# Kernel tuning notes

Hardware: AMD Instinct MI355X
Metric: run time of the kernel (lower is better)

## Reference

```python
import jax, jax.numpy as jnp
import numpy as np

B, S, D, H = 2, 2048, 1024, 16
HD = D // H


def setup_inputs() -> dict:
    key = jax.random.key(0)
    ks = jax.random.split(key, 7)
    mk = lambda k, shape, scale=1.0: (jax.random.normal(k, shape, dtype=jnp.float32) * scale)
    w_scale = 1.0 / np.sqrt(D)  # ~nn.Linear init scale
    return {
        "query": mk(ks[0], (B, S, D)),
        "key": mk(ks[1], (B, S, D)),
        "value": mk(ks[2], (B, S, D)),
        "Wq": mk(ks[3], (D, D), w_scale),
        "Wk": mk(ks[4], (D, D), w_scale),
        "Wv": mk(ks[5], (D, D), w_scale),
        "Wo": mk(ks[6], (D, D), w_scale),
    }


def reference(query, key, value, Wq, Wk, Wv, Wo):
    # torch nn.Linear(bias=False): y = x @ W.T, W is (out, in)
    def proj(x, W):
        y = jnp.einsum('bsd,ed->bse', x, W)          # [B, S, D]
        return y.reshape(x.shape[0], x.shape[1], H, HD).transpose(0, 2, 1, 3)  # [B, H, S, HD]

    Q = proj(query, Wq)
    K = proj(key, Wk)
    V = proj(value, Wv)

    # NOTE: original scales by sqrt(embedding_size), not sqrt(head_dim)
    scale = 1.0 / jnp.sqrt(jnp.asarray(D, dtype=Q.dtype))
    scores = jnp.einsum('bhqd,bhkd->bhqk', Q, K) * scale   # [B, H, Q, K]
    attn = jax.nn.softmax(scores, axis=-1)
    ctx = jnp.einsum('bhqk,bhkd->bhqd', attn, V)           # [B, H, Q, HD]
    ctx = ctx.transpose(0, 2, 1, 3).reshape(query.shape[0], query.shape[1], D)
    return jnp.einsum('bsd,ed->bse', ctx, Wo)
```

## Files before the change

### kernel.cpp

```cpp
#include <hip/hip_runtime.h>
#include <hip/hip_bf16.h>


typedef __bf16 bf16x8 __attribute__((ext_vector_type(8)));
typedef float f32x2 __attribute__((ext_vector_type(2)));
typedef float f32x4 __attribute__((ext_vector_type(4)));
typedef float f32x8 __attribute__((ext_vector_type(8)));
typedef float f32x16 __attribute__((ext_vector_type(16)));
typedef int i32x4 __attribute__((ext_vector_type(4)));

static constexpr int Bb = 2, Ss = 2048, Dd = 1024, Hh = 16, HDd = 64;
static constexpr int Mtot = Bb * Ss;

__global__ __launch_bounds__(256) void cast_all(
    const float* __restrict__ a0, const float* __restrict__ a1, const float* __restrict__ a2,
    const float* __restrict__ a3, const float* __restrict__ a4, const float* __restrict__ a5,
    const float* __restrict__ a6, __hip_bfloat16* __restrict__ d0, __hip_bfloat16* __restrict__ d1,
    __hip_bfloat16* __restrict__ d2, __hip_bfloat16* __restrict__ d3,
    __hip_bfloat16* __restrict__ d4, __hip_bfloat16* __restrict__ d5,
    __hip_bfloat16* __restrict__ d6, int nact8, int nw8) {
  const float* src;
  __hip_bfloat16* dst;
  int n8;
  switch (blockIdx.y) {
    case 0: src = a0; dst = d0; n8 = nact8; break;
    case 1: src = a1; dst = d1; n8 = nact8; break;
    case 2: src = a2; dst = d2; n8 = nact8; break;
    case 3: src = a3; dst = d3; n8 = nw8; break;
    case 4: src = a4; dst = d4; n8 = nw8; break;
    case 5: src = a5; dst = d5; n8 = nw8; break;
    default: src = a6; dst = d6; n8 = nw8; break;
  }
  int i = blockIdx.x * 256 + threadIdx.x;
  if (i >= n8) return;
  const float4* s4 = (const float4*)src + (size_t)i * 2;
  float4 a = s4[0], b = s4[1];
  union { __hip_bfloat16 h[8]; int4 v; } u;
  u.h[0] = __float2bfloat16(a.x); u.h[1] = __float2bfloat16(a.y);
  u.h[2] = __float2bfloat16(a.z); u.h[3] = __float2bfloat16(a.w);
  u.h[4] = __float2bfloat16(b.x); u.h[5] = __float2bfloat16(b.y);
  u.h[6] = __float2bfloat16(b.z); u.h[7] = __float2bfloat16(b.w);
  ((int4*)dst)[i] = u.v;
}

#define BM 128
#define BK 64

__device__ __forceinline__ void gload_lds16(const void* g, void* l) {
  __builtin_amdgcn_global_load_lds((const __attribute__((address_space(1))) unsigned*)g,
                                   (__attribute__((address_space(3))) unsigned*)l, 16, 0, 0);
}

__device__ __forceinline__ void storeC(float* C, size_t idx, float v) { C[idx] = v; }
__device__ __forceinline__ void storeC(__hip_bfloat16* C, size_t idx, float v) {
  C[idx] = __float2bfloat16(v);
}

template <typename OutT, int BNT>
__device__ __forceinline__ void gemm_bt_body(const __hip_bfloat16* __restrict__ A,
                                             const __hip_bfloat16* __restrict__ Bw,
                                             OutT* __restrict__ C, int K, int N, float cscale) {
  constexpr int NTC = BNT / 32;
  __shared__ __hip_bfloat16 As[BM * BK];
  __shared__ __hip_bfloat16 Bs[BNT * BK];
  const int tid = threadIdx.x;
  const int lane = tid & 63;
  const int wid = tid >> 6;
  const int wm = (wid >> 1) * 64;
  const int wn = (wid & 1) * (BNT / 2);
  const int bm = blockIdx.x, bn = blockIdx.y;
  const int l15 = lane & 15;
  const int lhi = lane >> 4;

  f32x4 zero = {0.f, 0.f, 0.f, 0.f};
  f32x4 acc[4][NTC];
#pragma unroll
  for (int i = 0; i < 4; ++i)
#pragma unroll
    for (int j = 0; j < NTC; ++j) acc[i][j] = zero;

  const size_t abase = (size_t)(bm * BM) * K;
  const size_t bbase = (size_t)(bn * BNT) * K;

  for (int k0 = 0; k0 < K; k0 += BK) {
#pragma unroll
    for (int p = 0; p < 4; ++p) {
      int c = p * 256 + tid;
      int row = c >> 3;
      int col = (c & 7) * 8;
      gload_lds16(A + abase + (size_t)row * K + k0 + col, (char*)As + c * 16);
    }
#pragma unroll
    for (int p = 0; p < BNT / 32; ++p) {
      int c = p * 256 + tid;
      int row = c >> 3;
      int col = (c & 7) * 8;
      gload_lds16(Bw + bbase + (size_t)row * K + k0 + col, (char*)Bs + c * 16);
    }
    __syncthreads();
#pragma unroll
    for (int kk = 0; kk < 2; ++kk) {
      bf16x8 af[4], bfr[NTC];
#pragma unroll
      for (int mt = 0; mt < 4; ++mt)
        af[mt] = *(const bf16x8*)&As[(wm + mt * 16 + l15) * BK + kk * 32 + lhi * 8];
#pragma unroll
      for (int nt = 0; nt < NTC; ++nt)
        bfr[nt] = *(const bf16x8*)&Bs[(wn + nt * 16 + l15) * BK + kk * 32 + lhi * 8];
#pragma unroll
      for (int mt = 0; mt < 4; ++mt)
#pragma unroll
        for (int nt = 0; nt < NTC; ++nt)
          acc[mt][nt] = __builtin_amdgcn_mfma_f32_16x16x32_bf16(af[mt], bfr[nt], acc[mt][nt], 0, 0, 0);
    }
    __syncthreads();
  }

#pragma unroll
  for (int mt = 0; mt < 4; ++mt)
#pragma unroll
    for (int r = 0; r < 4; ++r) {
      int row = bm * BM + wm + mt * 16 + lhi * 4 + r;
#pragma unroll
      for (int nt = 0; nt < NTC; ++nt) {
        int col = bn * BNT + wn + nt * 16 + l15;
        storeC(C, (size_t)row * N + col, acc[mt][nt][r] * cscale);
      }
    }
}

__global__ __launch_bounds__(256) void qkv_proj(
    const __hip_bfloat16* __restrict__ xq, const __hip_bfloat16* __restrict__ xk,
    const __hip_bfloat16* __restrict__ xv, const __hip_bfloat16* __restrict__ wq,
    const __hip_bfloat16* __restrict__ wk, const __hip_bfloat16* __restrict__ wv,
    __hip_bfloat16* __restrict__ Qp, __hip_bfloat16* __restrict__ Kp,
    __hip_bfloat16* __restrict__ Vp) {
  const __hip_bfloat16* A;
  const __hip_bfloat16* W;
  __hip_bfloat16* C;
  float cs = 1.0f;
  if (blockIdx.z == 0) { A = xq; W = wq; C = Qp; cs = 0.04508422f; }
  else if (blockIdx.z == 1) { A = xk; W = wk; C = Kp; }
  else { A = xv; W = wv; C = Vp; }
  gemm_bt_body<__hip_bfloat16, 128>(A, W, C, Dd, Dd, cs);
}

__global__ __launch_bounds__(256) void out_proj(const __hip_bfloat16* __restrict__ ctx,
                                                const __hip_bfloat16* __restrict__ wo,
                                                float* __restrict__ out) {
  gemm_bt_body<float, 64>(ctx, wo, out, Dd, Dd, 1.0f);
}

__global__ __launch_bounds__(256) void transpose_v(const __hip_bfloat16* __restrict__ Vp,
                                                   __hip_bfloat16* __restrict__ Vt) {
  __shared__ __hip_bfloat16 T[64][72];
  const int tid = threadIdx.x;
  const int s0 = blockIdx.x * 64;
  const int bh = blockIdx.y;
  const int b = bh >> 4, h = bh & 15;
  const __hip_bfloat16* src = Vp + (size_t)b * Ss * Dd + (size_t)h * HDd;
#pragma unroll
  for (int p = 0; p < 2; ++p) {
    int id = p * 256 + tid;
    int r = id >> 3, c8 = (id & 7) * 8;
    *(int4*)&T[r][c8] = *(const int4*)(src + (size_t)(s0 + r) * Dd + c8);
  }
  __syncthreads();
#pragma unroll
  for (int p = 0; p < 2; ++p) {
    int id = p * 256 + tid;
    int d = id >> 3, s8 = (id & 7) * 8;
    union { int4 v; __hip_bfloat16 hh[8]; } u;
#pragma unroll
    for (int j = 0; j < 8; ++j) u.hh[j] = T[s8 + j][d];
    *(int4*)(Vt + ((size_t)bh * HDd + d) * Ss + s0 + s8) = u.v;
  }
}

__global__ __launch_bounds__(256, 4) void attn_kernel(const __hip_bfloat16* __restrict__ Qp,
                                                      const __hip_bfloat16* __restrict__ Kp,
                                                      const __hip_bfloat16* __restrict__ Vt,
                                                      float* __restrict__ Po,
                                                      float* __restrict__ Pl) {
  constexpr int HT = 16;
  __shared__ __align__(16) __hip_bfloat16 Ks[2][64 * 64];
  __shared__ __align__(16) __hip_bfloat16 Vs[2][64 * 64];

  const int tid = threadIdx.x;
  const int lane = tid & 63, wid = tid >> 6;
  const int l31 = lane & 31;
  const bool hih = (lane >= 32);
  const int lhi2 = hih ? 1 : 0;

  const int bid = blockIdx.x;
  const int w = (bid & 7) * 128 + (bid >> 3);
  const int bh = w >> 5;
  const int qblk = (w & 31) >> 1;
  const int half = w & 1;

  const int b = bh >> 4, h = bh & 15;
  const size_t head_off = (size_t)b * Ss * Dd + (size_t)h * HDd;
  const size_t vt_off = (size_t)bh * HDd * Ss;
  const int qrow = qblk * 128 + wid * 32 + l31;

  bf16x8 qf[4];
#pragma unroll
  for (int ksd = 0; ksd < 4; ++ksd)
    qf[ksd] = *(const bf16x8*)(Qp + head_off + (size_t)qrow * Dd + ksd * 16 + lhi2 * 8);

  const i32x4 onesbits = {0x3F803F80, 0x3F803F80, 0x3F803F80, 0x3F803F80};
  const bf16x8 ones = __builtin_bit_cast(bf16x8, onesbits);

  f32x16 o[2], ol;
#pragma unroll
  for (int db = 0; db < 2; ++db)
#pragma unroll
    for (int r = 0; r < 16; ++r) o[db][r] = 0.f;
#pragma unroll
  for (int r = 0; r < 16; ++r) ol[r] = 0.f;

  auto stage_K = [&](int buf, int kv0) {
#pragma unroll
    for (int p = 0; p < 2; ++p) {
      int c = p * 256 + tid;
      int row = c >> 3;
      int sch = (c & 7) ^ (row & 7);
      gload_lds16(Kp + head_off + (size_t)(kv0 + row) * Dd + sch * 8,
                  (char*)&Ks[buf][0] + c * 16);
    }
  };
  auto stage_V = [&](int buf, int kv0) {
#pragma unroll
    for (int p = 0; p < 2; ++p) {
      int c = p * 256 + tid;
      int row = c >> 3;
      int sch = (c & 7) ^ (row & 7);
      gload_lds16(Vt + vt_off + (size_t)row * Ss + kv0 + sch * 8,
                  (char*)&Vs[buf][0] + c * 16);
    }
  };

  const int t0 = half * HT;
  stage_K(0, (t0 + 0) * 64);
  stage_V(0, (t0 + 0) * 64);
  stage_K(1, (t0 + 1) * 64);
  stage_V(1, (t0 + 1) * 64);
  asm volatile("s_waitcnt vmcnt(4)" ::: "memory");
  __builtin_amdgcn_s_barrier();
  __builtin_amdgcn_sched_barrier(0);

  for (int t = 0; t < HT; ++t) {
    const int cur = t & 1;
    if (t > 0 && t + 1 < HT) {
      stage_K(cur ^ 1, (t0 + t + 1) * 64);
      stage_V(cur ^ 1, (t0 + t + 1) * 64);
    }

    const char* kbase = (const char*)&Ks[cur][0];
    bf16x8 kfrag[2][4];
#pragma unroll
    for (int kb = 0; kb < 2; ++kb) {
      int row = kb * 32 + l31;
#pragma unroll
      for (int ksd = 0; ksd < 4; ++ksd)
        kfrag[kb][ksd] = *(const bf16x8*)(kbase + row * 128 +
                                          (((ksd * 2 + lhi2) ^ (row & 7)) << 4));
    }
    f32x16 st[2];
#pragma unroll
    for (int kb = 0; kb < 2; ++kb)
#pragma unroll
      for (int r = 0; r < 16; ++r) st[kb][r] = 0.f;
    __builtin_amdgcn_s_setprio(1);
#pragma unroll
    for (int kb = 0; kb < 2; ++kb)
#pragma unroll
      for (int ksd = 0; ksd < 4; ++ksd)
        st[kb] = __builtin_amdgcn_mfma_f32_32x32x16_bf16(kfrag[kb][ksd], qf[ksd], st[kb], 0, 0, 0);
    __builtin_amdgcn_s_setprio(0);

#pragma unroll
    for (int kb = 0; kb < 2; ++kb)
#pragma unroll
      for (int r = 0; r < 16; ++r) st[kb][r] = exp2f(st[kb][r]);

    int cpk[2][4][2];
#pragma unroll
    for (int kb = 0; kb < 2; ++kb)
#pragma unroll
      for (int g = 0; g < 4; ++g)
#pragma unroll
        for (int i = 0; i < 2; ++i) {
          int rr;
          float lo = st[kb][g * 4 + 2 * i], hi = st[kb][g * 4 + 2 * i + 1];
          asm("v_cvt_pk_bf16_f32 %0, %1, %2" : "=v"(rr) : "v"(lo), "v"(hi));
          cpk[kb][g][i] = rr;
        }

    if (t + 1 < HT) {
      asm volatile("s_waitcnt vmcnt(4)" ::: "memory");
    } else {
      asm volatile("s_waitcnt vmcnt(0)" ::: "memory");
    }

    const char* vbase = (const char*)&Vs[cur][0];
    bf16x8 vfrag[4][2];
#pragma unroll
    for (int ks = 0; ks < 4; ++ks)
#pragma unroll
      for (int db = 0; db < 2; ++db) {
        int row = db * 32 + l31;
        vfrag[ks][db] = *(const bf16x8*)(vbase + row * 128 +
                                         (((ks * 2 + lhi2) ^ (row & 7)) << 4));
      }
    __builtin_amdgcn_s_setprio(1);
#pragma unroll
    for (int ks = 0; ks < 4; ++ks) {
      const int kb = ks >> 1, m = ks & 1;
      int w0, w1, w2, w3;
#if __has_builtin(__builtin_amdgcn_permlane32_swap)
      {
        auto r0 = __builtin_amdgcn_permlane32_swap(cpk[kb][2 * m][0], cpk[kb][2 * m + 1][0],
                                                   false, false);
        auto r1 = __builtin_amdgcn_permlane32_swap(cpk[kb][2 * m][1], cpk[kb][2 * m + 1][1],
                                                   false, false);
        w0 = r0[0]; w2 = r0[1];
        w1 = r1[0]; w3 = r1[1];
      }
#else
      {
        int cA0 = cpk[kb][2 * m][0], cB0 = cpk[kb][2 * m + 1][0];
        int cA1 = cpk[kb][2 * m][1], cB1 = cpk[kb][2 * m + 1][1];
        int pay0 = hih ? cA0 : cB0, own0 = hih ? cB0 : cA0;
        int pay1 = hih ? cA1 : cB1, own1 = hih ? cB1 : cA1;
        int rcv0 = __shfl_xor(pay0, 32);
        int rcv1 = __shfl_xor(pay1, 32);
        w0 = hih ? rcv0 : own0;
        w1 = hih ? rcv1 : own1;
        w2 = hih ? own0 : rcv0;
        w3 = hih ? own1 : rcv1;
      }
#endif
      i32x4 bw = {w0, w1, w2, w3};
      bf16x8 pfrag = __builtin_bit_cast(bf16x8, bw);
#pragma unroll
      for (int db = 0; db < 2; ++db)
        o[db] = __builtin_amdgcn_mfma_f32_32x32x16_bf16(vfrag[ks][db], pfrag, o[db], 0, 0, 0);
      ol = __builtin_amdgcn_mfma_f32_32x32x16_bf16(ones, pfrag, ol, 0, 0, 0);
    }
    __builtin_amdgcn_s_setprio(0);

    if (t + 1 < HT) {
      asm volatile("s_waitcnt vmcnt(2)" ::: "memory");
      __builtin_amdgcn_s_barrier();
      __builtin_amdgcn_sched_barrier(0);
    }
  }

  const int qlocal = wid * 32 + l31;
  float* prow = Po + (size_t)w * (128 * 64) + (size_t)qlocal * 64;
#pragma unroll
  for (int db = 0; db < 2; ++db)
#pragma unroll
    for (int g = 0; g < 4; ++g) {
      f32x4 v4 = {o[db][g * 4 + 0], o[db][g * 4 + 1], o[db][g * 4 + 2], o[db][g * 4 + 3]};
      *(f32x4*)(prow + db * 32 + 8 * g + 4 * lhi2) = v4;
    }
  if (!hih) Pl[(size_t)w * 128 + qlocal] = ol[0];
}

__global__ __launch_bounds__(256) void merge_halves(const float* __restrict__ Po,
                                                    const float* __restrict__ Pl,
                                                    __hip_bfloat16* __restrict__ ctx) {
  const int mb = blockIdx.x;
  const int bh = mb >> 4, qblk = mb & 15;
  const int b = bh >> 4, h = bh & 15;
  const int tid = threadIdx.x;
  const int q = tid >> 1;
  const int dh = (tid & 1) * 32;
  const size_t w0 = (size_t)bh * 32 + qblk * 2;
  const float* p0 = Po + w0 * (128 * 64) + (size_t)q * 64 + dh;
  const float* p1 = p0 + 128 * 64;
  float l = Pl[w0 * 128 + q] + Pl[w0 * 128 + 128 + q];
  float inv = 1.f / l;
  __hip_bfloat16* dst =
      ctx + (size_t)b * Ss * Dd + (size_t)(qblk * 128 + q) * Dd + h * HDd + dh;
#pragma unroll
  for (int j = 0; j < 32; j += 4) {
    f32x4 a = *(const f32x4*)(p0 + j);
    f32x4 c = *(const f32x4*)(p1 + j);
    f32x4 s = (a + c) * inv;
    union { uint2 v; __hip_bfloat16 hh[4]; } u;
#pragma unroll
    for (int k = 0; k < 4; ++k) u.hh[k] = __float2bfloat16(s[k]);
    *(uint2*)(dst + j) = u.v;
  }
}

extern "C" void kernel_launch(void* const* d_in, const int* in_sizes, int n_in,
                              void* d_out, int out_size, void* d_ws, size_t ws_size,
                              hipStream_t stream) {
  const float* q_f = (const float*)d_in[0];
  const float* k_f = (const float*)d_in[1];
  const float* v_f = (const float*)d_in[2];
  const float* wq_f = (const float*)d_in[3];
  const float* wk_f = (const float*)d_in[4];
  const float* wv_f = (const float*)d_in[5];
  const float* wo_f = (const float*)d_in[6];
  float* out = (float*)d_out;

  const size_t act = (size_t)Mtot * Dd;
  const size_t wsz = (size_t)Dd * Dd;
  char* ws = (char*)d_ws;

  __hip_bfloat16* Qp = (__hip_bfloat16*)ws;   ws += act * 2;
  __hip_bfloat16* Kp = (__hip_bfloat16*)ws;   ws += act * 2;
  __hip_bfloat16* Vt = (__hip_bfloat16*)ws;   ws += act * 2;
  __hip_bfloat16* ctxb = (__hip_bfloat16*)ws; ws += act * 2;
  __hip_bfloat16* wob = (__hip_bfloat16*)ws;  ws += wsz * 2;

  char* scratch = ws;
  __hip_bfloat16* qb = (__hip_bfloat16*)scratch;
  __hip_bfloat16* kb = qb + act;
  __hip_bfloat16* vb = kb + act;
  __hip_bfloat16* wqb = vb + act;
  __hip_bfloat16* wkb = wqb + wsz;
  __hip_bfloat16* wvb = wkb + wsz;
  __hip_bfloat16* Vp = wvb + wsz;

  float* Po = (float*)scratch;
  float* Pl = Po + (size_t)1024 * 128 * 64;

  dim3 gc((unsigned)(act / 8 / 256), 7);
  cast_all<<<gc, 256, 0, stream>>>(q_f, k_f, v_f, wq_f, wk_f, wv_f, wo_f, qb, kb, vb, wqb,
                                   wkb, wvb, wob, (int)(act / 8), (int)(wsz / 8));

  dim3 gq(Mtot / BM, Dd / 128, 3);
  qkv_proj<<<gq, 256, 0, stream>>>(qb, kb, vb, wqb, wkb, wvb, Qp, Kp, Vp);

  dim3 gt(Ss / 64, Bb * Hh);
  transpose_v<<<gt, 256, 0, stream>>>(Vp, Vt);

  attn_kernel<<<1024, 256, 0, stream>>>(Qp, Kp, Vt, Po, Pl);

  merge_halves<<<512, 256, 0, stream>>>(Po, Pl, ctxb);

  dim3 go(Mtot / BM, Dd / 64);
  out_proj<<<go, 256, 0, stream>>>(ctxb, wob, out);
}
```

Baseline: 158.7 us.

## Fuse V transpose into QKV epilogue and merge-halves into output projection

The V projection epilogue now writes directly in the transposed per-head layout, which removes the separate transpose kernel and the Vp buffer. The split-KV merge (sum of the two halves and normalisation) is folded into the A-tile load of the output projection, so the merge kernel and the ctx buffer go away. The attention kernel also seeds its first MFMA with a zero register instead of zeroing the score accumulators. The trade-off is that every output-projection block column re-reads and re-normalises fp32 partials, with synchronous loads in place of async LDS loads, which greatly raises the read traffic for that GEMM.

```diff
diff --git a/kernel.cpp b/kernel.cpp
--- a/kernel.cpp
+++ b/kernel.cpp
@@ -56,7 +56,7 @@
   C[idx] = __float2bfloat16(v);
 }
 
-template <typename OutT, int BNT>
+template <typename OutT, int BNT, bool VT>
 __device__ __forceinline__ void gemm_bt_body(const __hip_bfloat16* __restrict__ A,
                                              const __hip_bfloat16* __restrict__ Bw,
                                              OutT* __restrict__ C, int K, int N, float cscale) {
@@ -116,17 +116,36 @@
     __syncthreads();
   }
 
-#pragma unroll
-  for (int mt = 0; mt < 4; ++mt)
-#pragma unroll
-    for (int r = 0; r < 4; ++r) {
-      int row = bm * BM + wm + mt * 16 + lhi * 4 + r;
+  if constexpr (VT) {
+    const int b = bm >> 4;
+    const int sbase = (bm & 15) * 128 + wm;
+#pragma unroll
+    for (int mt = 0; mt < 4; ++mt) {
+      int s0 = sbase + mt * 16 + lhi * 4;
 #pragma unroll
       for (int nt = 0; nt < NTC; ++nt) {
         int col = bn * BNT + wn + nt * 16 + l15;
-        storeC(C, (size_t)row * N + col, acc[mt][nt][r] * cscale);
-      }
-    }
+        int bh = b * 16 + (col >> 6);
+        int hd = col & 63;
+        union { uint2 v; __hip_bfloat16 hh[4]; } u;
+#pragma unroll
+        for (int r = 0; r < 4; ++r) u.hh[r] = __float2bfloat16(acc[mt][nt][r] * cscale);
+        *(uint2*)((__hip_bfloat16*)C + ((size_t)bh * 64 + hd) * (size_t)Ss + s0) = u.v;
+      }
+    }
+  } else {
+#pragma unroll
+    for (int mt = 0; mt < 4; ++mt)
+#pragma unroll
+      for (int r = 0; r < 4; ++r) {
+        int row = bm * BM + wm + mt * 16 + lhi * 4 + r;
+#pragma unroll
+        for (int nt = 0; nt < NTC; ++nt) {
+          int col = bn * BNT + wn + nt * 16 + l15;
+          storeC(C, (size_t)row * N + col, acc[mt][nt][r] * cscale);
+        }
+      }
+  }
 }
 
 __global__ __launch_bounds__(256) void qkv_proj(
@@ -134,47 +153,104 @@
     const __hip_bfloat16* __restrict__ xv, const __hip_bfloat16* __restrict__ wq,
     const __hip_bfloat16* __restrict__ wk, const __hip_bfloat16* __restrict__ wv,
     __hip_bfloat16* __restrict__ Qp, __hip_bfloat16* __restrict__ Kp,
-    __hip_bfloat16* __restrict__ Vp) {
-  const __hip_bfloat16* A;
-  const __hip_bfloat16* W;
-  __hip_bfloat16* C;
-  float cs = 1.0f;
-  if (blockIdx.z == 0) { A = xq; W = wq; C = Qp; cs = 0.04508422f; }
-  else if (blockIdx.z == 1) { A = xk; W = wk; C = Kp; }
-  else { A = xv; W = wv; C = Vp; }
-  gemm_bt_body<__hip_bfloat16, 128>(A, W, C, Dd, Dd, cs);
-}
-
-__global__ __launch_bounds__(256) void out_proj(const __hip_bfloat16* __restrict__ ctx,
-                                                const __hip_bfloat16* __restrict__ wo,
-                                                float* __restrict__ out) {
-  gemm_bt_body<float, 64>(ctx, wo, out, Dd, Dd, 1.0f);
-}
-
-__global__ __launch_bounds__(256) void transpose_v(const __hip_bfloat16* __restrict__ Vp,
-                                                   __hip_bfloat16* __restrict__ Vt) {
-  __shared__ __hip_bfloat16 T[64][72];
+    __hip_bfloat16* __restrict__ Vt) {
+  if (blockIdx.z == 0) {
+    gemm_bt_body<__hip_bfloat16, 128, false>(xq, wq, Qp, Dd, Dd, 0.04508422f);
+  } else if (blockIdx.z == 1) {
+    gemm_bt_body<__hip_bfloat16, 128, false>(xk, wk, Kp, Dd, Dd, 1.0f);
+  } else {
+    gemm_bt_body<__hip_bfloat16, 128, true>(xv, wv, Vt, Dd, Dd, 1.0f);
+  }
+}
+
+__global__ __launch_bounds__(256) void out_proj_fused(const float* __restrict__ Po,
+                                                      const float* __restrict__ Pl,
+                                                      const __hip_bfloat16* __restrict__ Bw,
+                                                      float* __restrict__ out) {
+  constexpr int BNT = 64;
+  __shared__ __hip_bfloat16 As[BM * BK];
+  __shared__ __hip_bfloat16 Bs[BNT * BK];
   const int tid = threadIdx.x;
-  const int s0 = blockIdx.x * 64;
-  const int bh = blockIdx.y;
-  const int b = bh >> 4, h = bh & 15;
-  const __hip_bfloat16* src = Vp + (size_t)b * Ss * Dd + (size_t)h * HDd;
-#pragma unroll
-  for (int p = 0; p < 2; ++p) {
-    int id = p * 256 + tid;
-    int r = id >> 3, c8 = (id & 7) * 8;
-    *(int4*)&T[r][c8] = *(const int4*)(src + (size_t)(s0 + r) * Dd + c8);
-  }
-  __syncthreads();
-#pragma unroll
-  for (int p = 0; p < 2; ++p) {
-    int id = p * 256 + tid;
-    int d = id >> 3, s8 = (id & 7) * 8;
-    union { int4 v; __hip_bfloat16 hh[8]; } u;
-#pragma unroll
-    for (int j = 0; j < 8; ++j) u.hh[j] = T[s8 + j][d];
-    *(int4*)(Vt + ((size_t)bh * HDd + d) * Ss + s0 + s8) = u.v;
-  }
+  const int lane = tid & 63;
+  const int wid = tid >> 6;
+  const int wm = (wid >> 1) * 64;
+  const int wn = (wid & 1) * 32;
+  const int bm = blockIdx.x, bn = blockIdx.y;
+  const int l15 = lane & 15;
+  const int lhi = lane >> 4;
+  const int b = bm >> 4, qblk = bm & 15;
+
+  f32x4 zero = {0.f, 0.f, 0.f, 0.f};
+  f32x4 acc[4][2];
+#pragma unroll
+  for (int i = 0; i < 4; ++i)
+#pragma unroll
+    for (int j = 0; j < 2; ++j) acc[i][j] = zero;
+
+  const size_t bbase = (size_t)(bn * BNT) * Dd;
+
+  for (int k0 = 0, hh = 0; k0 < Dd; k0 += BK, ++hh) {
+    const size_t w0 = (size_t)(b * 16 + hh) * 32 + qblk * 2;
+#pragma unroll
+    for (int p = 0; p < 4; ++p) {
+      int c = p * 256 + tid;
+      int row = c >> 3;
+      int col8 = (c & 7) * 8;
+      const float* p0 = Po + w0 * 8192 + (size_t)row * 64 + col8;
+      const float* p1 = p0 + 8192;
+      float l = Pl[w0 * 128 + row] + Pl[w0 * 128 + 128 + row];
+      float inv = 1.f / l;
+      f32x4 a0 = *(const f32x4*)p0;
+      f32x4 a1 = *(const f32x4*)(p0 + 4);
+      f32x4 c0 = *(const f32x4*)p1;
+      f32x4 c1 = *(const f32x4*)(p1 + 4);
+      f32x4 s0 = (a0 + c0) * inv;
+      f32x4 s1 = (a1 + c1) * inv;
+      union { int4 v; __hip_bfloat16 hh8[8]; } u;
+#pragma unroll
+      for (int j = 0; j < 4; ++j) {
+        u.hh8[j] = __float2bfloat16(s0[j]);
+        u.hh8[4 + j] = __float2bfloat16(s1[j]);
+      }
+      *(int4*)((char*)As + c * 16) = u.v;
+    }
+#pragma unroll
+    for (int p = 0; p < 2; ++p) {
+      int c = p * 256 + tid;
+      int row = c >> 3;
+      int col = (c & 7) * 8;
+      gload_lds16(Bw + bbase + (size_t)row * Dd + k0 + col, (char*)Bs + c * 16);
+    }
+    __syncthreads();
+#pragma unroll
+    for (int kk = 0; kk < 2; ++kk) {
+      bf16x8 af[4], bfr[2];
+#pragma unroll
+      for (int mt = 0; mt < 4; ++mt)
+        af[mt] = *(const bf16x8*)&As[(wm + mt * 16 + l15) * BK + kk * 32 + lhi * 8];
+#pragma unroll
+      for (int nt = 0; nt < 2; ++nt)
+        bfr[nt] = *(const bf16x8*)&Bs[(wn + nt * 16 + l15) * BK + kk * 32 + lhi * 8];
+#pragma unroll
+      for (int mt = 0; mt < 4; ++mt)
+#pragma unroll
+        for (int nt = 0; nt < 2; ++nt)
+          acc[mt][nt] = __builtin_amdgcn_mfma_f32_16x16x32_bf16(af[mt], bfr[nt], acc[mt][nt], 0, 0, 0);
+    }
+    __syncthreads();
+  }
+
+#pragma unroll
+  for (int mt = 0; mt < 4; ++mt)
+#pragma unroll
+    for (int r = 0; r < 4; ++r) {
+      int row = bm * BM + wm + mt * 16 + lhi * 4 + r;
+#pragma unroll
+      for (int nt = 0; nt < 2; ++nt) {
+        int col = bn * BNT + wn + nt * 16 + l15;
+        out[(size_t)row * Dd + col] = acc[mt][nt][r];
+      }
+    }
 }
 
 __global__ __launch_bounds__(256, 4) void attn_kernel(const __hip_bfloat16* __restrict__ Qp,
@@ -211,13 +287,9 @@
   const i32x4 onesbits = {0x3F803F80, 0x3F803F80, 0x3F803F80, 0x3F803F80};
   const bf16x8 ones = __builtin_bit_cast(bf16x8, onesbits);
 
-  f32x16 o[2], ol;
-#pragma unroll
-  for (int db = 0; db < 2; ++db)
-#pragma unroll
-    for (int r = 0; r < 16; ++r) o[db][r] = 0.f;
-#pragma unroll
-  for (int r = 0; r < 16; ++r) ol[r] = 0.f;
+  f32x16 o[2], ol, fz;
+#pragma unroll
+  for (int r = 0; r < 16; ++r) { o[0][r] = 0.f; o[1][r] = 0.f; ol[r] = 0.f; fz[r] = 0.f; }
 
   auto stage_K = [&](int buf, int kv0) {
 #pragma unroll
@@ -267,16 +339,14 @@
                                           (((ksd * 2 + lhi2) ^ (row & 7)) << 4));
     }
     f32x16 st[2];
-#pragma unroll
-    for (int kb = 0; kb < 2; ++kb)
-#pragma unroll
-      for (int r = 0; r < 16; ++r) st[kb][r] = 0.f;
     __builtin_amdgcn_s_setprio(1);
 #pragma unroll
-    for (int kb = 0; kb < 2; ++kb)
-#pragma unroll
-      for (int ksd = 0; ksd < 4; ++ksd)
+    for (int kb = 0; kb < 2; ++kb) {
+      st[kb] = __builtin_amdgcn_mfma_f32_32x32x16_bf16(kfrag[kb][0], qf[0], fz, 0, 0, 0);
+#pragma unroll
+      for (int ksd = 1; ksd < 4; ++ksd)
         st[kb] = __builtin_amdgcn_mfma_f32_32x32x16_bf16(kfrag[kb][ksd], qf[ksd], st[kb], 0, 0, 0);
+    }
     __builtin_amdgcn_s_setprio(0);
 
 #pragma unroll
@@ -369,34 +439,6 @@
   if (!hih) Pl[(size_t)w * 128 + qlocal] = ol[0];
 }
 
-__global__ __launch_bounds__(256) void merge_halves(const float* __restrict__ Po,
-                                                    const float* __restrict__ Pl,
-                                                    __hip_bfloat16* __restrict__ ctx) {
-  const int mb = blockIdx.x;
-  const int bh = mb >> 4, qblk = mb & 15;
-  const int b = bh >> 4, h = bh & 15;
-  const int tid = threadIdx.x;
-  const int q = tid >> 1;
-  const int dh = (tid & 1) * 32;
-  const size_t w0 = (size_t)bh * 32 + qblk * 2;
-  const float* p0 = Po + w0 * (128 * 64) + (size_t)q * 64 + dh;
-  const float* p1 = p0 + 128 * 64;
-  float l = Pl[w0 * 128 + q] + Pl[w0 * 128 + 128 + q];
-  float inv = 1.f / l;
-  __hip_bfloat16* dst =
-      ctx + (size_t)b * Ss * Dd + (size_t)(qblk * 128 + q) * Dd + h * HDd + dh;
-#pragma unroll
-  for (int j = 0; j < 32; j += 4) {
-    f32x4 a = *(const f32x4*)(p0 + j);
-    f32x4 c = *(const f32x4*)(p1 + j);
-    f32x4 s = (a + c) * inv;
-    union { uint2 v; __hip_bfloat16 hh[4]; } u;
-#pragma unroll
-    for (int k = 0; k < 4; ++k) u.hh[k] = __float2bfloat16(s[k]);
-    *(uint2*)(dst + j) = u.v;
-  }
-}
-
 extern "C" void kernel_launch(void* const* d_in, const int* in_sizes, int n_in,
                               void* d_out, int out_size, void* d_ws, size_t ws_size,
                               hipStream_t stream) {
@@ -416,7 +458,6 @@
   __hip_bfloat16* Qp = (__hip_bfloat16*)ws;   ws += act * 2;
   __hip_bfloat16* Kp = (__hip_bfloat16*)ws;   ws += act * 2;
   __hip_bfloat16* Vt = (__hip_bfloat16*)ws;   ws += act * 2;
-  __hip_bfloat16* ctxb = (__hip_bfloat16*)ws; ws += act * 2;
   __hip_bfloat16* wob = (__hip_bfloat16*)ws;  ws += wsz * 2;
 
   char* scratch = ws;
@@ -426,7 +467,6 @@
   __hip_bfloat16* wqb = vb + act;
   __hip_bfloat16* wkb = wqb + wsz;
   __hip_bfloat16* wvb = wkb + wsz;
-  __hip_bfloat16* Vp = wvb + wsz;
 
   float* Po = (float*)scratch;
   float* Pl = Po + (size_t)1024 * 128 * 64;
@@ -436,15 +476,10 @@
                                    wkb, wvb, wob, (int)(act / 8), (int)(wsz / 8));
 
   dim3 gq(Mtot / BM, Dd / 128, 3);
-  qkv_proj<<<gq, 256, 0, stream>>>(qb, kb, vb, wqb, wkb, wvb, Qp, Kp, Vp);
-
-  dim3 gt(Ss / 64, Bb * Hh);
-  transpose_v<<<gt, 256, 0, stream>>>(Vp, Vt);
+  qkv_proj<<<gq, 256, 0, stream>>>(qb, kb, vb, wqb, wkb, wvb, Qp, Kp, Vt);
 
   attn_kernel<<<1024, 256, 0, stream>>>(Qp, Kp, Vt, Po, Pl);
 
-  merge_halves<<<512, 256, 0, stream>>>(Po, Pl, ctxb);
-
   dim3 go(Mtot / BM, Dd / 64);
-  out_proj<<<go, 256, 0, stream>>>(ctxb, wob, out);
-}
+  out_proj_fused<<<go, 256, 0, stream>>>(Po, Pl, wob, out);
+}
```

New measurement: 180.0 us. 13.4% more time.

## Fuse activation fp32-to-bf16 cast into QKV projection and swizzle GEMM block order

Applied to the files above, without the earlier changes.

The three fp32 activations are no longer cast to bf16 by a separate kernel. The QKV projection GEMM now loads them as fp32 into registers, converts them, and writes the bf16 values to LDS, so a full bf16 write and re-read of the activations is avoided. The QKV and output projection grids are flattened into 1D and remapped with an XCD-style block swizzle to improve L2 locality. The attention kernel seeds the first QK MFMA with a zero vector instead of zero-initialising the accumulators separately. In exchange, the A tile now goes through registers rather than direct global-to-LDS loads, which can add latency and register pressure.

```diff
diff --git a/kernel.cpp b/kernel.cpp
--- a/kernel.cpp
+++ b/kernel.cpp
@@ -5,31 +5,32 @@
 typedef __bf16 bf16x8 __attribute__((ext_vector_type(8)));
 typedef float f32x2 __attribute__((ext_vector_type(2)));
 typedef float f32x4 __attribute__((ext_vector_type(4)));
-typedef float f32x8 __attribute__((ext_vector_type(8)));
 typedef float f32x16 __attribute__((ext_vector_type(16)));
 typedef int i32x4 __attribute__((ext_vector_type(4)));
 
 static constexpr int Bb = 2, Ss = 2048, Dd = 1024, Hh = 16, HDd = 64;
 static constexpr int Mtot = Bb * Ss;
 
-__global__ __launch_bounds__(256) void cast_all(
+#define BM 128
+#define BK 64
+
+__device__ __forceinline__ void gload_lds16(const void* g, void* l) {
+  __builtin_amdgcn_global_load_lds((const __attribute__((address_space(1))) unsigned*)g,
+                                   (__attribute__((address_space(3))) unsigned*)l, 16, 0, 0);
+}
+
+__global__ __launch_bounds__(256) void cast_w(
     const float* __restrict__ a0, const float* __restrict__ a1, const float* __restrict__ a2,
-    const float* __restrict__ a3, const float* __restrict__ a4, const float* __restrict__ a5,
-    const float* __restrict__ a6, __hip_bfloat16* __restrict__ d0, __hip_bfloat16* __restrict__ d1,
-    __hip_bfloat16* __restrict__ d2, __hip_bfloat16* __restrict__ d3,
-    __hip_bfloat16* __restrict__ d4, __hip_bfloat16* __restrict__ d5,
-    __hip_bfloat16* __restrict__ d6, int nact8, int nw8) {
+    const float* __restrict__ a3, __hip_bfloat16* __restrict__ d0,
+    __hip_bfloat16* __restrict__ d1, __hip_bfloat16* __restrict__ d2,
+    __hip_bfloat16* __restrict__ d3, int n8) {
   const float* src;
   __hip_bfloat16* dst;
-  int n8;
   switch (blockIdx.y) {
-    case 0: src = a0; dst = d0; n8 = nact8; break;
-    case 1: src = a1; dst = d1; n8 = nact8; break;
-    case 2: src = a2; dst = d2; n8 = nact8; break;
-    case 3: src = a3; dst = d3; n8 = nw8; break;
-    case 4: src = a4; dst = d4; n8 = nw8; break;
-    case 5: src = a5; dst = d5; n8 = nw8; break;
-    default: src = a6; dst = d6; n8 = nw8; break;
+    case 0: src = a0; dst = d0; break;
+    case 1: src = a1; dst = d1; break;
+    case 2: src = a2; dst = d2; break;
+    default: src = a3; dst = d3; break;
   }
   int i = blockIdx.x * 256 + threadIdx.x;
   if (i >= n8) return;
@@ -43,74 +44,85 @@
   ((int4*)dst)[i] = u.v;
 }
 
-#define BM 128
-#define BK 64
-
-__device__ __forceinline__ void gload_lds16(const void* g, void* l) {
-  __builtin_amdgcn_global_load_lds((const __attribute__((address_space(1))) unsigned*)g,
-                                   (__attribute__((address_space(3))) unsigned*)l, 16, 0, 0);
-}
-
-__device__ __forceinline__ void storeC(float* C, size_t idx, float v) { C[idx] = v; }
-__device__ __forceinline__ void storeC(__hip_bfloat16* C, size_t idx, float v) {
-  C[idx] = __float2bfloat16(v);
-}
-
-template <typename OutT, int BNT>
-__device__ __forceinline__ void gemm_bt_body(const __hip_bfloat16* __restrict__ A,
-                                             const __hip_bfloat16* __restrict__ Bw,
-                                             OutT* __restrict__ C, int K, int N, float cscale) {
-  constexpr int NTC = BNT / 32;
+__global__ __launch_bounds__(256) void qkv_proj(
+    const float* __restrict__ xq, const float* __restrict__ xk, const float* __restrict__ xv,
+    const __hip_bfloat16* __restrict__ wq, const __hip_bfloat16* __restrict__ wk,
+    const __hip_bfloat16* __restrict__ wv, __hip_bfloat16* __restrict__ Qp,
+    __hip_bfloat16* __restrict__ Kp, __hip_bfloat16* __restrict__ Vp) {
+  const int bid = blockIdx.x;
+  const int wsw = (bid & 7) * 96 + (bid >> 3);
+  const int arm = wsw >> 8;
+  const int rem = wsw & 255;
+  const int bm = rem >> 3, bn = rem & 7;
+
+  const float* Af = (arm == 0) ? xq : (arm == 1) ? xk : xv;
+  const __hip_bfloat16* Bw = (arm == 0) ? wq : (arm == 1) ? wk : wv;
+  __hip_bfloat16* C = (arm == 0) ? Qp : (arm == 1) ? Kp : Vp;
+  const float cscale = (arm == 0) ? 0.04508422f : 1.0f;
+
   __shared__ __hip_bfloat16 As[BM * BK];
-  __shared__ __hip_bfloat16 Bs[BNT * BK];
+  __shared__ __hip_bfloat16 Bs[BM * BK];
   const int tid = threadIdx.x;
   const int lane = tid & 63;
   const int wid = tid >> 6;
   const int wm = (wid >> 1) * 64;
-  const int wn = (wid & 1) * (BNT / 2);
-  const int bm = blockIdx.x, bn = blockIdx.y;
+  const int wn = (wid & 1) * 64;
   const int l15 = lane & 15;
   const int lhi = lane >> 4;
 
   f32x4 zero = {0.f, 0.f, 0.f, 0.f};
-  f32x4 acc[4][NTC];
+  f32x4 acc[4][4];
 #pragma unroll
   for (int i = 0; i < 4; ++i)
 #pragma unroll
-    for (int j = 0; j < NTC; ++j) acc[i][j] = zero;
-
-  const size_t abase = (size_t)(bm * BM) * K;
-  const size_t bbase = (size_t)(bn * BNT) * K;
-
-  for (int k0 = 0; k0 < K; k0 += BK) {
+    for (int j = 0; j < 4; ++j) acc[i][j] = zero;
+
+  const size_t abase = (size_t)(bm * BM) * Dd;
+  const size_t bbase = (size_t)(bn * BM) * Dd;
+
+  for (int k0 = 0; k0 < Dd; k0 += BK) {
+    f32x4 areg[4][2];
+#pragma unroll
+    for (int p = 0; p < 4; ++p) {
+      int c = p * 256 + tid;
+      int row = c >> 3;
+      int col8 = (c & 7) * 8;
+      const float* src = Af + abase + (size_t)row * Dd + k0 + col8;
+      areg[p][0] = *(const f32x4*)src;
+      areg[p][1] = *(const f32x4*)(src + 4);
+    }
 #pragma unroll
     for (int p = 0; p < 4; ++p) {
       int c = p * 256 + tid;
       int row = c >> 3;
       int col = (c & 7) * 8;
-      gload_lds16(A + abase + (size_t)row * K + k0 + col, (char*)As + c * 16);
-    }
-#pragma unroll
-    for (int p = 0; p < BNT / 32; ++p) {
-      int c = p * 256 + tid;
-      int row = c >> 3;
-      int col = (c & 7) * 8;
-      gload_lds16(Bw + bbase + (size_t)row * K + k0 + col, (char*)Bs + c * 16);
+      gload_lds16(Bw + bbase + (size_t)row * Dd + k0 + col, (char*)Bs + c * 16);
+    }
+#pragma unroll
+    for (int p = 0; p < 4; ++p) {
+      int c = p * 256 + tid;
+      union { int4 v; __hip_bfloat16 h[8]; } u;
+#pragma unroll
+      for (int j = 0; j < 4; ++j) {
+        u.h[j] = __float2bfloat16(areg[p][0][j]);
+        u.h[4 + j] = __float2bfloat16(areg[p][1][j]);
+      }
+      *(int4*)((char*)As + c * 16) = u.v;
     }
     __syncthreads();
 #pragma unroll
     for (int kk = 0; kk < 2; ++kk) {
-      bf16x8 af[4], bfr[NTC];
+      bf16x8 af[4], bfr[4];
 #pragma unroll
       for (int mt = 0; mt < 4; ++mt)
         af[mt] = *(const bf16x8*)&As[(wm + mt * 16 + l15) * BK + kk * 32 + lhi * 8];
 #pragma unroll
-      for (int nt = 0; nt < NTC; ++nt)
+      for (int nt = 0; nt < 4; ++nt)
         bfr[nt] = *(const bf16x8*)&Bs[(wn + nt * 16 + l15) * BK + kk * 32 + lhi * 8];
 #pragma unroll
       for (int mt = 0; mt < 4; ++mt)
 #pragma unroll
-        for (int nt = 0; nt < NTC; ++nt)
+        for (int nt = 0; nt < 4; ++nt)
           acc[mt][nt] = __builtin_amdgcn_mfma_f32_16x16x32_bf16(af[mt], bfr[nt], acc[mt][nt], 0, 0, 0);
     }
     __syncthreads();
@@ -122,33 +134,11 @@
     for (int r = 0; r < 4; ++r) {
       int row = bm * BM + wm + mt * 16 + lhi * 4 + r;
 #pragma unroll
-      for (int nt = 0; nt < NTC; ++nt) {
-        int col = bn * BNT + wn + nt * 16 + l15;
-        storeC(C, (size_t)row * N + col, acc[mt][nt][r] * cscale);
+      for (int nt = 0; nt < 4; ++nt) {
+        int col = bn * BM + wn + nt * 16 + l15;
+        C[(size_t)row * Dd + col] = __float2bfloat16(acc[mt][nt][r] * cscale);
       }
     }
-}
-
-__global__ __launch_bounds__(256) void qkv_proj(
-    const __hip_bfloat16* __restrict__ xq, const __hip_bfloat16* __restrict__ xk,
-    const __hip_bfloat16* __restrict__ xv, const __hip_bfloat16* __restrict__ wq,
-    const __hip_bfloat16* __restrict__ wk, const __hip_bfloat16* __restrict__ wv,
-    __hip_bfloat16* __restrict__ Qp, __hip_bfloat16* __restrict__ Kp,
-    __hip_bfloat16* __restrict__ Vp) {
-  const __hip_bfloat16* A;
-  const __hip_bfloat16* W;
-  __hip_bfloat16* C;
-  float cs = 1.0f;
-  if (blockIdx.z == 0) { A = xq; W = wq; C = Qp; cs = 0.04508422f; }
-  else if (blockIdx.z == 1) { A = xk; W = wk; C = Kp; }
-  else { A = xv; W = wv; C = Vp; }
-  gemm_bt_body<__hip_bfloat16, 128>(A, W, C, Dd, Dd, cs);
-}
-
-__global__ __launch_bounds__(256) void out_proj(const __hip_bfloat16* __restrict__ ctx,
-                                                const __hip_bfloat16* __restrict__ wo,
-                                                float* __restrict__ out) {
-  gemm_bt_body<float, 64>(ctx, wo, out, Dd, Dd, 1.0f);
 }
 
 __global__ __launch_bounds__(256) void transpose_v(const __hip_bfloat16* __restrict__ Vp,
@@ -211,13 +201,9 @@
   const i32x4 onesbits = {0x3F803F80, 0x3F803F80, 0x3F803F80, 0x3F803F80};
   const bf16x8 ones = __builtin_bit_cast(bf16x8, onesbits);
 
-  f32x16 o[2], ol;
-#pragma unroll
-  for (int db = 0; db < 2; ++db)
-#pragma unroll
-    for (int r = 0; r < 16; ++r) o[db][r] = 0.f;
-#pragma unroll
-  for (int r = 0; r < 16; ++r) ol[r] = 0.f;
+  f32x16 o[2], ol, fz;
+#pragma unroll
+  for (int r = 0; r < 16; ++r) { o[0][r] = 0.f; o[1][r] = 0.f; ol[r] = 0.f; fz[r] = 0.f; }
 
   auto stage_K = [&](int buf, int kv0) {
 #pragma unroll
@@ -267,16 +253,14 @@
                                           (((ksd * 2 + lhi2) ^ (row & 7)) << 4));
     }
     f32x16 st[2];
-#pragma unroll
-    for (int kb = 0; kb < 2; ++kb)
-#pragma unroll
-      for (int r = 0; r < 16; ++r) st[kb][r] = 0.f;
     __builtin_amdgcn_s_setprio(1);
 #pragma unroll
-    for (int kb = 0; kb < 2; ++kb)
-#pragma unroll
-      for (int ksd = 0; ksd < 4; ++ksd)
+    for (int kb = 0; kb < 2; ++kb) {
+      st[kb] = __builtin_amdgcn_mfma_f32_32x32x16_bf16(kfrag[kb][0], qf[0], fz, 0, 0, 0);
+#pragma unroll
+      for (int ksd = 1; ksd < 4; ++ksd)
         st[kb] = __builtin_amdgcn_mfma_f32_32x32x16_bf16(kfrag[kb][ksd], qf[ksd], st[kb], 0, 0, 0);
+    }
     __builtin_amdgcn_s_setprio(0);
 
 #pragma unroll
@@ -397,6 +381,80 @@
   }
 }
 
+__global__ __launch_bounds__(256) void out_proj(const __hip_bfloat16* __restrict__ A,
+                                                const __hip_bfloat16* __restrict__ Bw,
+                                                float* __restrict__ out) {
+  constexpr int BNT = 64;
+  __shared__ __hip_bfloat16 As[BM * BK];
+  __shared__ __hip_bfloat16 Bs[BNT * BK];
+  const int bid = blockIdx.x;
+  const int wsw = (bid & 7) * 64 + (bid >> 3);
+  const int bm = wsw >> 4, bn = wsw & 15;
+  const int tid = threadIdx.x;
+  const int lane = tid & 63;
+  const int wid = tid >> 6;
+  const int wm = (wid >> 1) * 64;
+  const int wn = (wid & 1) * 32;
+  const int l15 = lane & 15;
+  const int lhi = lane >> 4;
+
+  f32x4 zero = {0.f, 0.f, 0.f, 0.f};
+  f32x4 acc[4][2];
+#pragma unroll
+  for (int i = 0; i < 4; ++i)
+#pragma unroll
+    for (int j = 0; j < 2; ++j) acc[i][j] = zero;
+
+  const size_t abase = (size_t)(bm * BM) * Dd;
+  const size_t bbase = (size_t)(bn * BNT) * Dd;
+
+  for (int k0 = 0; k0 < Dd; k0 += BK) {
+#pragma unroll
+    for (int p = 0; p < 4; ++p) {
+      int c = p * 256 + tid;
+      int row = c >> 3;
+      int col = (c & 7) * 8;
+      gload_lds16(A + abase + (size_t)row * Dd + k0 + col, (char*)As + c * 16);
+    }
+#pragma unroll
+    for (int p = 0; p < 2; ++p) {
+      int c = p * 256 + tid;
+      int row = c >> 3;
+      int col = (c & 7) * 8;
+      gload_lds16(Bw + bbase + (size_t)row * Dd + k0 + col, (char*)Bs + c * 16);
+    }
+    __syncthreads();
+#pragma unroll
+    for (int kk = 0; kk < 2; ++kk) {
+      bf16x8 af[4], bfr[2];
+#pragma unroll
+      for (int mt = 0; mt < 4; ++mt)
+        af[mt] = *(const bf16x8*)&As[(wm + mt * 16 + l15) * BK + kk * 32 + lhi * 8];
+#pragma unroll
+      for (int nt = 0; nt < 2; ++nt)
+        bfr[nt] = *(const bf16x8*)&Bs[(wn + nt * 16 + l15) * BK + kk * 32 + lhi * 8];
+#pragma unroll
+      for (int mt = 0; mt < 4; ++mt)
+#pragma unroll
+        for (int nt = 0; nt < 2; ++nt)
+          acc[mt][nt] = __builtin_amdgcn_mfma_f32_16x16x32_bf16(af[mt], bfr[nt], acc[mt][nt], 0, 0, 0);
+    }
+    __syncthreads();
+  }
+
+#pragma unroll
+  for (int mt = 0; mt < 4; ++mt)
+#pragma unroll
+    for (int r = 0; r < 4; ++r) {
+      int row = bm * BM + wm + mt * 16 + lhi * 4 + r;
+#pragma unroll
+      for (int nt = 0; nt < 2; ++nt) {
+        int col = bn * BNT + wn + nt * 16 + l15;
+        out[(size_t)row * Dd + col] = acc[mt][nt][r];
+      }
+    }
+}
+
 extern "C" void kernel_launch(void* const* d_in, const int* in_sizes, int n_in,
                               void* d_out, int out_size, void* d_ws, size_t ws_size,
                               hipStream_t stream) {
@@ -420,10 +478,7 @@
   __hip_bfloat16* wob = (__hip_bfloat16*)ws;  ws += wsz * 2;
 
   char* scratch = ws;
-  __hip_bfloat16* qb = (__hip_bfloat16*)scratch;
-  __hip_bfloat16* kb = qb + act;
-  __hip_bfloat16* vb = kb + act;
-  __hip_bfloat16* wqb = vb + act;
+  __hip_bfloat16* wqb = (__hip_bfloat16*)scratch;
   __hip_bfloat16* wkb = wqb + wsz;
   __hip_bfloat16* wvb = wkb + wsz;
   __hip_bfloat16* Vp = wvb + wsz;
@@ -431,12 +486,10 @@
   float* Po = (float*)scratch;
   float* Pl = Po + (size_t)1024 * 128 * 64;
 
-  dim3 gc((unsigned)(act / 8 / 256), 7);
-  cast_all<<<gc, 256, 0, stream>>>(q_f, k_f, v_f, wq_f, wk_f, wv_f, wo_f, qb, kb, vb, wqb,
-                                   wkb, wvb, wob, (int)(act / 8), (int)(wsz / 8));
-
-  dim3 gq(Mtot / BM, Dd / 128, 3);
-  qkv_proj<<<gq, 256, 0, stream>>>(qb, kb, vb, wqb, wkb, wvb, Qp, Kp, Vp);
+  dim3 gc((unsigned)(wsz / 8 / 256), 4);
+  cast_w<<<gc, 256, 0, stream>>>(wq_f, wk_f, wv_f, wo_f, wqb, wkb, wvb, wob, (int)(wsz / 8));
+
+  qkv_proj<<<768, 256, 0, stream>>>(q_f, k_f, v_f, wqb, wkb, wvb, Qp, Kp, Vp);
 
   dim3 gt(Ss / 64, Bb * Hh);
   transpose_v<<<gt, 256, 0, stream>>>(Vp, Vt);
@@ -445,6 +498,5 @@
 
   merge_halves<<<512, 256, 0, stream>>>(Po, Pl, ctxb);
 
-  dim3 go(Mtot / BM, Dd / 64);
-  out_proj<<<go, 256, 0, stream>>>(ctxb, wob, out);
-}
+  out_proj<<<512, 256, 0, stream>>>(ctxb, wob, out);
+}
```

Result: no change. 160.8 us (+1.3%).

## Split attention KV range four ways and swizzle out-projection block order

Applied to the files above, without the earlier changes.

The attention kernel now takes a runtime split count, so each query block's KV range is divided across four workgroups instead of two when workspace allows. This gives 2048 blocks for more parallelism and shorter per-block loops. The merge kernel is generalized to sum a variable number of partials, which doubles the partial-output traffic. Out-projection blocks are remapped with an XCD-style swizzle for cache locality. The first QK MFMA now uses a zero accumulator instead of explicit zeroing, and the occupancy hint in launch_bounds is dropped, which may change register allocation.

```diff
diff --git a/kernel.cpp b/kernel.cpp
--- a/kernel.cpp
+++ b/kernel.cpp
@@ -5,7 +5,6 @@
 typedef __bf16 bf16x8 __attribute__((ext_vector_type(8)));
 typedef float f32x2 __attribute__((ext_vector_type(2)));
 typedef float f32x4 __attribute__((ext_vector_type(4)));
-typedef float f32x8 __attribute__((ext_vector_type(8)));
 typedef float f32x16 __attribute__((ext_vector_type(16)));
 typedef int i32x4 __attribute__((ext_vector_type(4)));
 
@@ -59,7 +58,8 @@
 template <typename OutT, int BNT>
 __device__ __forceinline__ void gemm_bt_body(const __hip_bfloat16* __restrict__ A,
                                              const __hip_bfloat16* __restrict__ Bw,
-                                             OutT* __restrict__ C, int K, int N, float cscale) {
+                                             OutT* __restrict__ C, int K, int N, float cscale,
+                                             int bm, int bn) {
   constexpr int NTC = BNT / 32;
   __shared__ __hip_bfloat16 As[BM * BK];
   __shared__ __hip_bfloat16 Bs[BNT * BK];
@@ -68,7 +68,6 @@
   const int wid = tid >> 6;
   const int wm = (wid >> 1) * 64;
   const int wn = (wid & 1) * (BNT / 2);
-  const int bm = blockIdx.x, bn = blockIdx.y;
   const int l15 = lane & 15;
   const int lhi = lane >> 4;
 
@@ -142,13 +141,16 @@
   if (blockIdx.z == 0) { A = xq; W = wq; C = Qp; cs = 0.04508422f; }
   else if (blockIdx.z == 1) { A = xk; W = wk; C = Kp; }
   else { A = xv; W = wv; C = Vp; }
-  gemm_bt_body<__hip_bfloat16, 128>(A, W, C, Dd, Dd, cs);
+  gemm_bt_body<__hip_bfloat16, 128>(A, W, C, Dd, Dd, cs, blockIdx.x, blockIdx.y);
 }
 
 __global__ __launch_bounds__(256) void out_proj(const __hip_bfloat16* __restrict__ ctx,
                                                 const __hip_bfloat16* __restrict__ wo,
                                                 float* __restrict__ out) {
-  gemm_bt_body<float, 64>(ctx, wo, out, Dd, Dd, 1.0f);
+  const int bid = blockIdx.x;
+  const int wsw = (bid & 7) * 64 + (bid >> 3);
+  const int bm = wsw >> 4, bn = wsw & 15;
+  gemm_bt_body<float, 64>(ctx, wo, out, Dd, Dd, 1.0f, bm, bn);
 }
 
 __global__ __launch_bounds__(256) void transpose_v(const __hip_bfloat16* __restrict__ Vp,
@@ -177,12 +179,11 @@
   }
 }
 
-__global__ __launch_bounds__(256, 4) void attn_kernel(const __hip_bfloat16* __restrict__ Qp,
-                                                      const __hip_bfloat16* __restrict__ Kp,
-                                                      const __hip_bfloat16* __restrict__ Vt,
-                                                      float* __restrict__ Po,
-                                                      float* __restrict__ Pl) {
-  constexpr int HT = 16;
+__global__ __launch_bounds__(256) void attn_kernel(const __hip_bfloat16* __restrict__ Qp,
+                                                   const __hip_bfloat16* __restrict__ Kp,
+                                                   const __hip_bfloat16* __restrict__ Vt,
+                                                   float* __restrict__ Po,
+                                                   float* __restrict__ Pl, int ls) {
   __shared__ __align__(16) __hip_bfloat16 Ks[2][64 * 64];
   __shared__ __align__(16) __hip_bfloat16 Vs[2][64 * 64];
 
@@ -193,10 +194,14 @@
   const int lhi2 = hih ? 1 : 0;
 
   const int bid = blockIdx.x;
-  const int w = (bid & 7) * 128 + (bid >> 3);
-  const int bh = w >> 5;
-  const int qblk = (w & 31) >> 1;
-  const int half = w & 1;
+  const int chunk = gridDim.x >> 3;
+  const int w = (bid & 7) * chunk + (bid >> 3);
+  const int nsplit = 1 << ls;
+  const int half = w & (nsplit - 1);
+  const int rest = w >> ls;
+  const int qblk = rest & 15;
+  const int bh = rest >> 4;
+  const int HT = 32 >> ls;
 
   const int b = bh >> 4, h = bh & 15;
   const size_t head_off = (size_t)b * Ss * Dd + (size_t)h * HDd;
@@ -211,13 +216,9 @@
   const i32x4 onesbits = {0x3F803F80, 0x3F803F80, 0x3F803F80, 0x3F803F80};
   const bf16x8 ones = __builtin_bit_cast(bf16x8, onesbits);
 
-  f32x16 o[2], ol;
-#pragma unroll
-  for (int db = 0; db < 2; ++db)
-#pragma unroll
-    for (int r = 0; r < 16; ++r) o[db][r] = 0.f;
-#pragma unroll
-  for (int r = 0; r < 16; ++r) ol[r] = 0.f;
+  f32x16 o[2], ol, fz;
+#pragma unroll
+  for (int r = 0; r < 16; ++r) { o[0][r] = 0.f; o[1][r] = 0.f; ol[r] = 0.f; fz[r] = 0.f; }
 
   auto stage_K = [&](int buf, int kv0) {
 #pragma unroll
@@ -267,16 +268,14 @@
                                           (((ksd * 2 + lhi2) ^ (row & 7)) << 4));
     }
     f32x16 st[2];
-#pragma unroll
-    for (int kb = 0; kb < 2; ++kb)
-#pragma unroll
-      for (int r = 0; r < 16; ++r) st[kb][r] = 0.f;
     __builtin_amdgcn_s_setprio(1);
 #pragma unroll
-    for (int kb = 0; kb < 2; ++kb)
-#pragma unroll
-      for (int ksd = 0; ksd < 4; ++ksd)
+    for (int kb = 0; kb < 2; ++kb) {
+      st[kb] = __builtin_amdgcn_mfma_f32_32x32x16_bf16(kfrag[kb][0], qf[0], fz, 0, 0, 0);
+#pragma unroll
+      for (int ksd = 1; ksd < 4; ++ksd)
         st[kb] = __builtin_amdgcn_mfma_f32_32x32x16_bf16(kfrag[kb][ksd], qf[ksd], st[kb], 0, 0, 0);
+    }
     __builtin_amdgcn_s_setprio(0);
 
 #pragma unroll
@@ -371,29 +370,30 @@
 
 __global__ __launch_bounds__(256) void merge_halves(const float* __restrict__ Po,
                                                     const float* __restrict__ Pl,
-                                                    __hip_bfloat16* __restrict__ ctx) {
+                                                    __hip_bfloat16* __restrict__ ctx,
+                                                    int nsplit) {
   const int mb = blockIdx.x;
   const int bh = mb >> 4, qblk = mb & 15;
   const int b = bh >> 4, h = bh & 15;
   const int tid = threadIdx.x;
   const int q = tid >> 1;
   const int dh = (tid & 1) * 32;
-  const size_t w0 = (size_t)bh * 32 + qblk * 2;
-  const float* p0 = Po + w0 * (128 * 64) + (size_t)q * 64 + dh;
-  const float* p1 = p0 + 128 * 64;
-  float l = Pl[w0 * 128 + q] + Pl[w0 * 128 + 128 + q];
+  const size_t w0 = ((size_t)bh * 16 + qblk) * nsplit;
+  float l = 0.f;
+  for (int j = 0; j < nsplit; ++j) l += Pl[(w0 + j) * 128 + q];
   float inv = 1.f / l;
   __hip_bfloat16* dst =
       ctx + (size_t)b * Ss * Dd + (size_t)(qblk * 128 + q) * Dd + h * HDd + dh;
 #pragma unroll
-  for (int j = 0; j < 32; j += 4) {
-    f32x4 a = *(const f32x4*)(p0 + j);
-    f32x4 c = *(const f32x4*)(p1 + j);
-    f32x4 s = (a + c) * inv;
+  for (int jj = 0; jj < 32; jj += 4) {
+    f32x4 s = {0.f, 0.f, 0.f, 0.f};
+    for (int j = 0; j < nsplit; ++j)
+      s += *(const f32x4*)(Po + (w0 + j) * 8192 + (size_t)q * 64 + dh + jj);
+    s *= inv;
     union { uint2 v; __hip_bfloat16 hh[4]; } u;
 #pragma unroll
     for (int k = 0; k < 4; ++k) u.hh[k] = __float2bfloat16(s[k]);
-    *(uint2*)(dst + j) = u.v;
+    *(uint2*)(dst + jj) = u.v;
   }
 }
 
@@ -418,6 +418,13 @@
   __hip_bfloat16* Vt = (__hip_bfloat16*)ws;   ws += act * 2;
   __hip_bfloat16* ctxb = (__hip_bfloat16*)ws; ws += act * 2;
   __hip_bfloat16* wob = (__hip_bfloat16*)ws;  ws += wsz * 2;
+  const size_t persistent = (size_t)(ws - (char*)d_ws);
+
+  int ls = 2, nsplit = 4;
+  {
+    size_t po4 = (size_t)2048 * 8192 * 4 + (size_t)2048 * 128 * 4;
+    if (ws_size < persistent + po4) { ls = 1; nsplit = 2; }
+  }
 
   char* scratch = ws;
   __hip_bfloat16* qb = (__hip_bfloat16*)scratch;
@@ -429,7 +436,7 @@
   __hip_bfloat16* Vp = wvb + wsz;
 
   float* Po = (float*)scratch;
-  float* Pl = Po + (size_t)1024 * 128 * 64;
+  float* Pl = Po + (size_t)512 * nsplit * 128 * 64;
 
   dim3 gc((unsigned)(act / 8 / 256), 7);
   cast_all<<<gc, 256, 0, stream>>>(q_f, k_f, v_f, wq_f, wk_f, wv_f, wo_f, qb, kb, vb, wqb,
@@ -441,10 +448,9 @@
   dim3 gt(Ss / 64, Bb * Hh);
   transpose_v<<<gt, 256, 0, stream>>>(Vp, Vt);
 
-  attn_kernel<<<1024, 256, 0, stream>>>(Qp, Kp, Vt, Po, Pl);
-
-  merge_halves<<<512, 256, 0, stream>>>(Po, Pl, ctxb);
-
-  dim3 go(Mtot / BM, Dd / 64);
-  out_proj<<<go, 256, 0, stream>>>(ctxb, wob, out);
-}
+  attn_kernel<<<512 * nsplit, 256, 0, stream>>>(Qp, Kp, Vt, Po, Pl, ls);
+
+  merge_halves<<<512, 256, 0, stream>>>(Po, Pl, ctxb, nsplit);
+
+  out_proj<<<512, 256, 0, stream>>>(ctxb, wob, out);
+}
```

Result: slower. 246.1 us (+55.1%).
